# Kernel optimization log

Measured on AMD Instinct MI355X. Metric: run time of the kernel, lower is better.

Reference implementation:

```python
import jax, jax.numpy as jnp
import numpy as np
from jax import lax

WINDOW = 512
HOP = 128
SR = 16000
ALPHA = 1e-06
F = WINDOW // 2 + 1  # 257 bins
GAIN = float(np.sqrt(8.0 / 3.0))

# frequency-domain constants (match PsychoacousticMasker properties)
_freqs = np.linspace(0.0, SR / 2.0, F)
_bark_np = 13.0 * np.arctan(0.00076 * _freqs) + 3.5 * np.arctan((_freqs / 7500.0) ** 2)
_valid_dom = (_freqs >= 20.0) & (_freqs <= 20000.0)
_ath_np = np.full(F, -np.inf)
_fk = _freqs[_valid_dom] * 0.001
_ath_np[_valid_dom] = 3.64 * _fk ** -0.8 - 6.5 * np.exp(-0.6 * (_fk - 3.3) ** 2) + 0.001 * _fk ** 4 - 12.0
BARK = jnp.asarray(_bark_np, jnp.float32)
ATH = jnp.asarray(_ath_np, jnp.float32)
DELTA_SHIFT = -6.025 - 0.275 * BARK
HANN = jnp.asarray(0.5 * (1.0 - np.cos(2.0 * np.pi * np.arange(WINDOW) / WINDOW)), jnp.float32)


def _stft(x):
    # center=False hann STFT -> [n_frames, F] complex
    n_frames = (x.shape[0] - WINDOW) // HOP + 1
    idx = jnp.arange(n_frames)[:, None] * HOP + jnp.arange(WINDOW)[None, :]
    return jnp.fft.rfft(x[idx] * HANN, axis=-1)


def _frame_threshold(p):
    # p: [F] SPL-normalized PSD (dB) for one frame -> global masking threshold [F]
    interior = (p[1:-1] > p[:-2]) & (p[1:-1] > p[2:])
    is_max = jnp.pad(interior, (1, 1), constant_values=False)
    pw = 10.0 ** (p / 10.0)
    m_all = 10.0 * jnp.log10(pw + jnp.roll(pw, 1) + jnp.roll(pw, -1))  # tonal masker level (bins j-1,j,j+1)
    valid = is_max & (m_all > ATH)
    order = jnp.argsort((~valid).astype(jnp.int32))  # stable: valid bins first, in frequency order
    vmask = valid[order]
    m_c = jnp.where(vmask, m_all[order], -200.0)     # compacted masker dB values
    n = valid.sum()

    def step(carry, i):
        i_prev, keep = carry
        active = i < n
        # NB: source indexes bark[] with masker *list positions* (i, i_prev); replicated faithfully
        close = (BARK[i] - BARK[i_prev]) < 0.5
        prev_smaller = m_c[i_prev] < m_c[i]
        del_idx = jnp.where(prev_smaller, i_prev, i)
        keep = jnp.where(active & close, keep.at[del_idx].set(False), keep)
        i_prev = jnp.where(active, jnp.where(close, jnp.where(prev_smaller, i_prev + 1, i_prev), i), i_prev)
        return (i_prev, keep), None

    (_, keep), _ = lax.scan(step, (jnp.int32(0), jnp.ones(F, dtype=bool)), jnp.arange(1, F, dtype=jnp.int32))
    keep = keep & vmask
    # individual thresholds, vectorized over maskers k and bins
    z_j = BARK[order]                                    # bark of each masker's bin
    dz = BARK[None, :] - z_j[:, None]                    # [K, F]
    slope = jnp.where(dz > 0, -27.0 + 0.37 * jnp.maximum(m_c - 40.0, 0.0)[:, None], 27.0)
    t = m_c[:, None] + DELTA_SHIFT[order][:, None] + slope * dz
    power = jnp.where(keep[:, None], 10.0 ** (t / 10.0), 0.0)
    return 10.0 * jnp.log10(power.sum(0) + 10.0 ** (ATH / 10.0))


def _threshold_and_psd_max(audio):
    s = _stft(audio)                                     # [T, F]
    psd = 20.0 * jnp.log10(jnp.abs(GAIN * s / WINDOW))
    psd = jnp.maximum(psd, -200.0)
    psd_max = psd.max()
    psd_n = 96.0 - psd_max + psd
    thr = jax.vmap(_frame_threshold)(psd_n)              # [T, F]
    return thr, psd_max


def setup_inputs() -> dict:
    key = jax.random.key(0)
    k1, k2 = jax.random.split(key)
    L = 160000  # 10 s @ 16 kHz; (L - 512) % 128 == 0 -> 1247 frames, pad is a no-op
    x_ref = 0.5 * jax.random.normal(k1, (L,), dtype=jnp.float32)
    x_adv = x_ref + 0.01 * jax.random.normal(k2, (L,), dtype=jnp.float32)
    return {"x_adv": x_adv, "x_ref": x_ref}


def reference(x_adv, x_ref):
    thr, psd_max = _threshold_and_psd_max(x_ref)
    thr = lax.stop_gradient(thr)
    psd_max = lax.stop_gradient(psd_max)
    delta = x_adv - x_ref
    sd = _stft(delta)                                    # [T, F]
    psd_d = (GAIN / WINDOW) ** 2 * (sd.real ** 2 + sd.imag ** 2)
    psd_d = (10.0 ** 9.6) / (10.0 ** (psd_max / 10.0)) * psd_d
    loss = jnp.mean(jax.nn.relu(psd_d - 10.0 ** (thr / 10.0)))
    return ALPHA * loss
```

## Files before the change

kernel.cpp:

```cpp
#include <hip/hip_runtime.h>
#include <math.h>


#define FBINS 257

#define TAB_BARK  0
#define TAB_ATHDB 257
#define TAB_ATHP  514
#define TAB_HANN  771
#define TAB_TWR   1283
#define TAB_TWI   1539
#define TAB_FLOATS 2048

__global__ __launch_bounds__(256) void k0_init(float* __restrict__ tab)
{
    const int tid = threadIdx.x;
    const double TWO_PI = 6.283185307179586476925286766559;
    if (blockIdx.x == 0) {
        for (int f = tid; f < FBINS; f += 256) {
            double freq = 31.25 * (double)f;
            double q    = freq / 7500.0;
            tab[TAB_BARK + f] = (float)(13.0 * atan(0.00076 * freq) + 3.5 * atan(q * q));
            if (f == 0) {
                tab[TAB_ATHDB] = -INFINITY;
                tab[TAB_ATHP]  = 0.0f;
            } else {
                double fk = freq * 0.001;
                double ad = 3.64 * pow(fk, -0.8)
                          - 6.5 * exp(-0.6 * (fk - 3.3) * (fk - 3.3))
                          + 0.001 * fk * fk * fk * fk - 12.0;
                float av = (float)ad;
                tab[TAB_ATHDB + f] = av;
                tab[TAB_ATHP  + f] = exp10f(av / 10.0f);
            }
        }
    } else if (blockIdx.x == 1) {
        for (int n = tid; n < 512; n += 256) {
            double cw = cos((TWO_PI * (double)n) / 512.0);
            tab[TAB_HANN + n] = (float)(0.5 * (1.0 - cw));
        }
    } else {
        for (int j = tid; j < 256; j += 256) {
            double s, c;
            sincos(-(TWO_PI / 512.0) * (double)j, &s, &c);
            tab[TAB_TWR + j] = (float)c;
            tab[TAB_TWI + j] = (float)s;
        }
    }
}

__global__ __launch_bounds__(256) void k1_stft(
    const float* __restrict__ xadv, const float* __restrict__ xref,
    const float* __restrict__ tab,
    float* __restrict__ psd_db, float* __restrict__ pd, float* __restrict__ fmaxs)
{
    __shared__ float re[2][512], im[2][512], twr[256], twi[256];
    __shared__ float wmax[4];
    const int t = blockIdx.x, tid = threadIdx.x;

    twr[tid] = tab[TAB_TWR + tid];
    twi[tid] = tab[TAB_TWI + tid];

    const int base_idx = t * 128;
    for (int n = tid; n < 512; n += 256) {
        float w = tab[TAB_HANN + n];
        float r = xref[base_idx + n];
        float a = xadv[base_idx + n];
        int   p = __brev((unsigned)n) >> 23;
        re[0][p] = w * r;
        im[0][p] = w * (a - r);
    }
    __syncthreads();

    int cur = 0;
    for (int stage = 1; stage <= 9; ++stage) {
        int half  = 1 << (stage - 1);
        int tstep = 512 >> stage;
        int j     = tid & (half - 1);
        int base  = ((tid >> (stage - 1)) << stage) + j;
        float wr = twr[j * tstep], wi = twi[j * tstep];
        float vr0 = re[cur][base + half], vi0 = im[cur][base + half];
        float vr = vr0 * wr - vi0 * wi;
        float vi = vr0 * wi + vi0 * wr;
        float ur = re[cur][base], ui = im[cur][base];
        re[cur ^ 1][base]        = ur + vr; im[cur ^ 1][base]        = ui + vi;
        re[cur ^ 1][base + half] = ur - vr; im[cur ^ 1][base + half] = ui - vi;
        cur ^= 1;
        __syncthreads();
    }

    const float S2 = 1.0172526041666667e-05f;
    float lmax = -1e30f;
    for (int k = tid; k <= 256; k += 256) {
        int nk = (512 - k) & 511;
        float zr = re[cur][k],  zi = im[cur][k];
        float yr = re[cur][nk], yi = im[cur][nk];
        float ar = 0.5f * (zr + yr), ai = 0.5f * (zi - yi);
        float br = 0.5f * (zi + yi), bi = 0.5f * (yr - zr);
        float prefp = S2 * (ar * ar + ai * ai);
        float pdb   = fmaxf(10.0f * log10f(prefp), -200.0f);
        psd_db[t * FBINS + k] = pdb;
        pd[t * FBINS + k]     = S2 * (br * br + bi * bi);
        lmax = fmaxf(lmax, pdb);
    }
    for (int off = 32; off > 0; off >>= 1) lmax = fmaxf(lmax, __shfl_down(lmax, off));
    if ((tid & 63) == 0) wmax[tid >> 6] = lmax;
    __syncthreads();
    if (tid == 0)
        fmaxs[t] = fmaxf(fmaxf(wmax[0], wmax[1]), fmaxf(wmax[2], wmax[3]));
}

__global__ __launch_bounds__(256) void k2_max(
    const float* __restrict__ fmaxs, int nf, float* __restrict__ psdmax)
{
    __shared__ float sm[4];
    float v = -1e30f;
    for (int i = threadIdx.x; i < nf; i += 256) v = fmaxf(v, fmaxs[i]);
    for (int off = 32; off > 0; off >>= 1) v = fmaxf(v, __shfl_down(v, off));
    if ((threadIdx.x & 63) == 0) sm[threadIdx.x >> 6] = v;
    __syncthreads();
    if (threadIdx.x == 0)
        psdmax[0] = fmaxf(fmaxf(sm[0], sm[1]), fmaxf(sm[2], sm[3]));
}

__global__ __launch_bounds__(256) void k3_threshold(
    const float* __restrict__ tab,
    const float* __restrict__ psd_db, const float* __restrict__ pd,
    const float* __restrict__ psdmax, float* __restrict__ floss)
{
    __shared__ float barkf[FBINS], athp_s[FBINS];
    __shared__ float p_s[FBINS], pw_s[FBINS];
    __shared__ float mc_s[128], shift_s[128], barkm_s[128], ups_s[128];
    __shared__ int   bin_s[128], keep_s[128];
    __shared__ float2 pmk[132];
    __shared__ int   wcnt[4];
    __shared__ float red[4];

    const int t = blockIdx.x, tid = threadIdx.x;
    const int lane = tid & 63, wid = tid >> 6;
    const float pmax   = psdmax[0];
    const float shift0 = 96.0f - pmax;

    for (int f = tid; f < FBINS; f += 256) {
        barkf[f]  = tab[TAB_BARK + f];
        athp_s[f] = tab[TAB_ATHP + f];
        float pv = shift0 + psd_db[t * FBINS + f];
        p_s[f]  = pv;
        pw_s[f] = exp10f(pv / 10.0f);
    }
    __syncthreads();

    float m = -1e30f;
    int   pred = 0;
    if (tid >= 1 && tid <= 255) {
        float pc = p_s[tid];
        if (pc > p_s[tid - 1] && pc > p_s[tid + 1]) {
            m = 10.0f * log10f((pw_s[tid] + pw_s[tid - 1]) + pw_s[tid + 1]);
            if (m > tab[TAB_ATHDB + tid]) pred = 1;
        }
    }
    unsigned long long bal = __ballot(pred);
    if (lane == 0) wcnt[wid] = __popcll(bal);
    __syncthreads();
    int base = 0;
    for (int w = 0; w < wid; ++w) base += wcnt[w];
    const int n_total = wcnt[0] + wcnt[1] + wcnt[2] + wcnt[3];
    if (pred) {
        int pos = base + __popcll(bal & ((1ull << lane) - 1));
        bin_s[pos] = tid; mc_s[pos] = m; keep_s[pos] = 1;
    }
    __syncthreads();

    if (tid <= n_total && tid < 130) {
        pmk[tid] = (tid < n_total) ? make_float2(barkf[tid], mc_s[tid])
                                   : make_float2(1.0e30f, -1.0e30f);
    }
    __syncthreads();

    if (tid == 0 && n_total > 1) {
        int   i_prev = 0;
        float bp = pmk[0].x, mp = pmk[0].y;
        float2 c = pmk[1];
        for (int i = 1; i < n_total; ++i) {
            float2 nx = pmk[i + 1];
            bool close        = (c.x - bp) < 0.5f;
            bool prev_smaller = mp < c.y;
            if (close) {
                keep_s[prev_smaller ? i_prev : i] = 0;
                if (prev_smaller) {
                    ++i_prev;
                    if (i_prev == i) { bp = c.x; mp = c.y; }
                    else { float2 p = pmk[i_prev]; bp = p.x; mp = p.y; }
                }
            } else {
                i_prev = i; bp = c.x; mp = c.y;
            }
            c = nx;
        }
    }
    __syncthreads();

    int pred2 = (tid < n_total) && keep_s[tid];
    unsigned long long bal2 = __ballot(pred2);
    if (lane == 0) wcnt[wid] = __popcll(bal2);
    __syncthreads();
    int base2 = 0;
    for (int w = 0; w < wid; ++w) base2 += wcnt[w];
    const int nk = wcnt[0] + wcnt[1] + wcnt[2] + wcnt[3];
    if (pred2) {
        int pos = base2 + __popcll(bal2 & ((1ull << lane) - 1));
        int   fb = bin_s[tid];
        float mc = mc_s[tid];
        shift_s[pos] = mc + (-6.025f - 0.275f * barkf[fb]);
        barkm_s[pos] = barkf[fb];
        ups_s[pos]   = -27.0f + 0.37f * fmaxf(mc - 40.0f, 0.0f);
    }
    __syncthreads();

    const float C = 3981071705.534973f / exp10f(pmax / 10.0f);
    float lsum = 0.0f;
    for (int f = tid; f < FBINS; f += 256) {
        float bf  = barkf[f];
        float acc = 0.0f;
        for (int k = 0; k < nk; ++k) {
            float dz    = bf - barkm_s[k];
            float slope = (dz > 0.0f) ? ups_s[k] : 27.0f;
            float tdb   = shift_s[k] + slope * dz;
            acc += exp10f(tdb / 10.0f);
        }
        float thrpow = acc + athp_s[f];
        float pds    = C * pd[t * FBINS + f];
        lsum += fmaxf(pds - thrpow, 0.0f);
    }
    for (int off = 32; off > 0; off >>= 1) lsum += __shfl_down(lsum, off);
    if ((tid & 63) == 0) red[tid >> 6] = lsum;
    __syncthreads();
    if (tid == 0) floss[t] = (red[0] + red[1]) + (red[2] + red[3]);
}

__global__ __launch_bounds__(256) void k4_final(
    const float* __restrict__ floss, int nf, float* __restrict__ out)
{
    __shared__ float red[4];
    float s = 0.0f;
    for (int i = threadIdx.x; i < nf; i += 256) s += floss[i];
    for (int off = 32; off > 0; off >>= 1) s += __shfl_down(s, off);
    if ((threadIdx.x & 63) == 0) red[threadIdx.x >> 6] = s;
    __syncthreads();
    if (threadIdx.x == 0) {
        float total = (red[0] + red[1]) + (red[2] + red[3]);
        out[0] = 1e-6f * (total / (float)(nf * FBINS));
    }
}

extern "C" void kernel_launch(void* const* d_in, const int* in_sizes, int n_in,
                              void* d_out, int out_size, void* d_ws, size_t ws_size,
                              hipStream_t stream)
{
    const float* x_adv = (const float*)d_in[0];
    const float* x_ref = (const float*)d_in[1];
    float*       out   = (float*)d_out;

    const int L  = in_sizes[0];
    const int nf = (L - 512) / 128 + 1;

    float* ws      = (float*)d_ws;
    float* tab     = ws;
    float* psd_db  = ws + TAB_FLOATS;
    float* pd      = psd_db + (size_t)nf * FBINS;
    float* fmaxs   = pd + (size_t)nf * FBINS;
    float* floss   = fmaxs + nf;
    float* psdmax  = floss + nf;

    k0_init     <<<3,  256, 0, stream>>>(tab);
    k1_stft     <<<nf, 256, 0, stream>>>(x_adv, x_ref, tab, psd_db, pd, fmaxs);
    k2_max      <<<1,  256, 0, stream>>>(fmaxs, nf, psdmax);
    k3_threshold<<<nf, 256, 0, stream>>>(tab, psd_db, pd, psdmax, floss);
    k4_final    <<<1,  256, 0, stream>>>(floss, nf, out);
}
```

Baseline: 89.25 us.

## Register-resident FFT with wave shuffles and fold global max into threshold kernel

The 512-point FFT now keeps each butterfly pair in registers. The first six stages exchange data through cross-lane shuffles, and only the last cross-wave stages go through shared memory. This removes most of the per-stage __syncthreads and LDS traffic. The separate max-reduction kernel is removed, and every threshold block now redundantly reduces the per-frame maxima itself. That saves one launch but adds about 1247 reads per block.

```diff
diff --git a/kernel.cpp b/kernel.cpp
--- a/kernel.cpp
+++ b/kernel.cpp
@@ -54,49 +54,92 @@
     const float* __restrict__ tab,
     float* __restrict__ psd_db, float* __restrict__ pd, float* __restrict__ fmaxs)
 {
-    __shared__ float re[2][512], im[2][512], twr[256], twi[256];
+    __shared__ float2 tw2[256];
+    __shared__ float2 bufA[256], bufB[256];
+    __shared__ float2 zf[512];
     __shared__ float wmax[4];
     const int t = blockIdx.x, tid = threadIdx.x;
 
-    twr[tid] = tab[TAB_TWR + tid];
-    twi[tid] = tab[TAB_TWI + tid];
+    tw2[tid] = make_float2(tab[TAB_TWR + tid], tab[TAB_TWI + tid]);
 
     const int base_idx = t * 128;
-    for (int n = tid; n < 512; n += 256) {
-        float w = tab[TAB_HANN + n];
-        float r = xref[base_idx + n];
-        float a = xadv[base_idx + n];
-        int   p = __brev((unsigned)n) >> 23;
-        re[0][p] = w * r;
-        im[0][p] = w * (a - r);
-    }
-    __syncthreads();
-
-    int cur = 0;
-    for (int stage = 1; stage <= 9; ++stage) {
-        int half  = 1 << (stage - 1);
-        int tstep = 512 >> stage;
-        int j     = tid & (half - 1);
-        int base  = ((tid >> (stage - 1)) << stage) + j;
-        float wr = twr[j * tstep], wi = twi[j * tstep];
-        float vr0 = re[cur][base + half], vi0 = im[cur][base + half];
-        float vr = vr0 * wr - vi0 * wi;
-        float vi = vr0 * wi + vi0 * wr;
-        float ur = re[cur][base], ui = im[cur][base];
-        re[cur ^ 1][base]        = ur + vr; im[cur ^ 1][base]        = ui + vi;
-        re[cur ^ 1][base + half] = ur - vr; im[cur ^ 1][base + half] = ui - vi;
-        cur ^= 1;
+    const int n0 = (int)(__brev((unsigned)tid) >> 24);
+    const int n1 = n0 + 256;
+    float w0 = tab[TAB_HANN + n0], w1 = tab[TAB_HANN + n1];
+    float r0 = xref[base_idx + n0], r1 = xref[base_idx + n1];
+    float a0 = xadv[base_idx + n0], a1 = xadv[base_idx + n1];
+    float2 E0 = make_float2(w0 * r0, w0 * (a0 - r0));
+    float2 E1 = make_float2(w1 * r1, w1 * (a1 - r1));
+    __syncthreads();
+
+    #pragma unroll
+    for (int s = 1; s <= 7; ++s) {
+        const int half  = 1 << (s - 1);
+        const int tstep = 512 >> s;
+        float2 w = tw2[(tid & (half - 1)) * tstep];
+        float vr = E1.x * w.x - E1.y * w.y;
+        float vi = E1.x * w.y + E1.y * w.x;
+        float ur = E0.x, ui = E0.y;
+        E0 = make_float2(ur + vr, ui + vi);
+        E1 = make_float2(ur - vr, ui - vi);
+        if (s <= 6) {
+            const int d = 1 << (s - 1);
+            int b = (tid >> (s - 1)) & 1;
+            float2 keep = b ? E1 : E0;
+            float2 send = b ? E0 : E1;
+            float2 recv;
+            recv.x = __shfl_xor(send.x, d);
+            recv.y = __shfl_xor(send.y, d);
+            E0 = b ? recv : keep;
+            E1 = b ? keep : recv;
+        }
+    }
+    {
+        int b = (tid >> 6) & 1;
+        float2 keep = b ? E1 : E0;
+        bufA[tid] = b ? E0 : E1;
         __syncthreads();
-    }
+        float2 recv = bufA[tid ^ 64];
+        E0 = b ? recv : keep;
+        E1 = b ? keep : recv;
+    }
+    {
+        float2 w = tw2[(tid & 127) * 2];
+        float vr = E1.x * w.x - E1.y * w.y;
+        float vi = E1.x * w.y + E1.y * w.x;
+        float ur = E0.x, ui = E0.y;
+        E0 = make_float2(ur + vr, ui + vi);
+        E1 = make_float2(ur - vr, ui - vi);
+    }
+    {
+        int b = (tid >> 7) & 1;
+        float2 keep = b ? E1 : E0;
+        bufB[tid] = b ? E0 : E1;
+        __syncthreads();
+        float2 recv = bufB[tid ^ 128];
+        E0 = b ? recv : keep;
+        E1 = b ? keep : recv;
+    }
+    {
+        float2 w = tw2[tid];
+        float vr = E1.x * w.x - E1.y * w.y;
+        float vi = E1.x * w.y + E1.y * w.x;
+        float ur = E0.x, ui = E0.y;
+        E0 = make_float2(ur + vr, ui + vi);
+        E1 = make_float2(ur - vr, ui - vi);
+    }
+    zf[tid]       = E0;
+    zf[tid + 256] = E1;
+    __syncthreads();
 
     const float S2 = 1.0172526041666667e-05f;
     float lmax = -1e30f;
     for (int k = tid; k <= 256; k += 256) {
         int nk = (512 - k) & 511;
-        float zr = re[cur][k],  zi = im[cur][k];
-        float yr = re[cur][nk], yi = im[cur][nk];
-        float ar = 0.5f * (zr + yr), ai = 0.5f * (zi - yi);
-        float br = 0.5f * (zi + yi), bi = 0.5f * (yr - zr);
+        float2 zk = zf[k];
+        float2 zn = zf[nk];
+        float ar = 0.5f * (zk.x + zn.x), ai = 0.5f * (zk.y - zn.y);
+        float br = 0.5f * (zk.y + zn.y), bi = 0.5f * (zn.x - zk.x);
         float prefp = S2 * (ar * ar + ai * ai);
         float pdb   = fmaxf(10.0f * log10f(prefp), -200.0f);
         psd_db[t * FBINS + k] = pdb;
@@ -110,23 +153,10 @@
         fmaxs[t] = fmaxf(fmaxf(wmax[0], wmax[1]), fmaxf(wmax[2], wmax[3]));
 }
 
-__global__ __launch_bounds__(256) void k2_max(
-    const float* __restrict__ fmaxs, int nf, float* __restrict__ psdmax)
-{
-    __shared__ float sm[4];
-    float v = -1e30f;
-    for (int i = threadIdx.x; i < nf; i += 256) v = fmaxf(v, fmaxs[i]);
-    for (int off = 32; off > 0; off >>= 1) v = fmaxf(v, __shfl_down(v, off));
-    if ((threadIdx.x & 63) == 0) sm[threadIdx.x >> 6] = v;
-    __syncthreads();
-    if (threadIdx.x == 0)
-        psdmax[0] = fmaxf(fmaxf(sm[0], sm[1]), fmaxf(sm[2], sm[3]));
-}
-
 __global__ __launch_bounds__(256) void k3_threshold(
     const float* __restrict__ tab,
     const float* __restrict__ psd_db, const float* __restrict__ pd,
-    const float* __restrict__ psdmax, float* __restrict__ floss)
+    const float* __restrict__ fmaxs, int nf, float* __restrict__ floss)
 {
     __shared__ float barkf[FBINS], athp_s[FBINS];
     __shared__ float p_s[FBINS], pw_s[FBINS];
@@ -135,18 +165,35 @@
     __shared__ float2 pmk[132];
     __shared__ int   wcnt[4];
     __shared__ float red[4];
+    __shared__ float sm[4];
 
     const int t = blockIdx.x, tid = threadIdx.x;
     const int lane = tid & 63, wid = tid >> 6;
-    const float pmax   = psdmax[0];
-    const float shift0 = 96.0f - pmax;
+
+    const float pdb_a = psd_db[t * FBINS + tid];
+    const float pdb_b = psd_db[t * FBINS + 256];
 
     for (int f = tid; f < FBINS; f += 256) {
         barkf[f]  = tab[TAB_BARK + f];
         athp_s[f] = tab[TAB_ATHP + f];
-        float pv = shift0 + psd_db[t * FBINS + f];
-        p_s[f]  = pv;
-        pw_s[f] = exp10f(pv / 10.0f);
+    }
+    float v = -1e30f;
+    for (int i = tid; i < nf; i += 256) v = fmaxf(v, fmaxs[i]);
+    for (int off = 32; off > 0; off >>= 1) v = fmaxf(v, __shfl_down(v, off));
+    if (lane == 0) sm[wid] = v;
+    __syncthreads();
+    const float pmax   = fmaxf(fmaxf(sm[0], sm[1]), fmaxf(sm[2], sm[3]));
+    const float shift0 = 96.0f - pmax;
+
+    {
+        float pv = shift0 + pdb_a;
+        p_s[tid]  = pv;
+        pw_s[tid] = exp10f(pv / 10.0f);
+        if (tid == 0) {
+            float pv2 = shift0 + pdb_b;
+            p_s[256]  = pv2;
+            pw_s[256] = exp10f(pv2 / 10.0f);
+        }
     }
     __syncthreads();
 
@@ -270,11 +317,9 @@
     float* pd      = psd_db + (size_t)nf * FBINS;
     float* fmaxs   = pd + (size_t)nf * FBINS;
     float* floss   = fmaxs + nf;
-    float* psdmax  = floss + nf;
 
     k0_init     <<<3,  256, 0, stream>>>(tab);
     k1_stft     <<<nf, 256, 0, stream>>>(x_adv, x_ref, tab, psd_db, pd, fmaxs);
-    k2_max      <<<1,  256, 0, stream>>>(fmaxs, nf, psdmax);
-    k3_threshold<<<nf, 256, 0, stream>>>(tab, psd_db, pd, psdmax, floss);
+    k3_threshold<<<nf, 256, 0, stream>>>(tab, psd_db, pd, fmaxs, nf, floss);
     k4_final    <<<1,  256, 0, stream>>>(floss, nf, out);
 }
```

Result: faster. 85.04 us (-4.7%).
